# Performance work log

Measured on AMD Instinct MI355X. Metric: run time of the kernel, lower is better.

Reference implementation:

```python
import jax, jax.numpy as jnp
import numpy as np

N_DEV, N_TASK, E = 50000, 100000, 1000000
F_DEV, F_TASK = 64, 64
HID, H, OUT = 16, 4, 32
L1 = HID * H  # 64


def gat_conv(x_src, x_dst, src, dst, W_src, W_dst, a_src, a_dst, b, heads, ch, n_dst):
    """PyG-style bipartite GATConv (concat=True, negative_slope=0.2, no self loops)."""
    hs = (x_src @ W_src).reshape(-1, heads, ch)          # [Ns,H,C]
    hd = (x_dst @ W_dst).reshape(-1, heads, ch)          # [Nd,H,C]
    al_s = jnp.sum(hs * a_src, axis=-1)                  # [Ns,H]
    al_d = jnp.sum(hd * a_dst, axis=-1)                  # [Nd,H]
    e = jax.nn.leaky_relu(al_s[src] + al_d[dst], 0.2)    # [E,H]
    m = jax.ops.segment_max(e, dst, num_segments=n_dst)  # [Nd,H]
    ex = jnp.exp(e - m[dst])
    den = jax.ops.segment_sum(ex, dst, num_segments=n_dst)
    attn = ex / (den[dst] + 1e-16)                       # [E,H]
    msg = attn[:, :, None] * hs[src]                     # [E,H,C]
    out = jax.ops.segment_sum(msg, dst, num_segments=n_dst)
    return out.reshape(n_dst, heads * ch) + b


def setup_inputs() -> dict:
    key = jax.random.key(0)
    ks = jax.random.split(key, 32)
    rn = lambda k, s: jax.random.normal(k, s, jnp.float32) * 0.1
    inp = {
        "x_dev": jax.random.normal(ks[0], (N_DEV, F_DEV), jnp.float32),
        "x_task": jax.random.normal(ks[1], (N_TASK, F_TASK), jnp.float32),
        "writes_src": jax.random.randint(ks[2], (E,), 0, N_DEV, jnp.int32),
        "writes_dst": jax.random.randint(ks[3], (E,), 0, N_TASK, jnp.int32),
        "wb_src": jax.random.randint(ks[4], (E,), 0, N_TASK, jnp.int32),
        "wb_dst": jax.random.randint(ks[5], (E,), 0, N_DEV, jnp.int32),
        # layer1: dev->task (src=dev, dst=task), H=4, C=16
        "W1a_src": rn(ks[6], (F_DEV, L1)), "W1a_dst": rn(ks[7], (F_TASK, L1)),
        "a1a_src": rn(ks[8], (H, HID)), "a1a_dst": rn(ks[9], (H, HID)),
        "b1a": jnp.zeros((L1,), jnp.float32),
        # layer1: task->dev
        "W1b_src": rn(ks[10], (F_TASK, L1)), "W1b_dst": rn(ks[11], (F_DEV, L1)),
        "a1b_src": rn(ks[12], (H, HID)), "a1b_dst": rn(ks[13], (H, HID)),
        "b1b": jnp.zeros((L1,), jnp.float32),
        # layer2: dev->task, heads=1, C=32
        "W2a_src": rn(ks[14], (L1, OUT)), "W2a_dst": rn(ks[15], (L1, OUT)),
        "a2a_src": rn(ks[16], (1, OUT)), "a2a_dst": rn(ks[17], (1, OUT)),
        "b2a": jnp.zeros((OUT,), jnp.float32),
        # layer2: task->dev
        "W2b_src": rn(ks[18], (L1, OUT)), "W2b_dst": rn(ks[19], (L1, OUT)),
        "a2b_src": rn(ks[20], (1, OUT)), "a2b_dst": rn(ks[21], (1, OUT)),
        "b2b": jnp.zeros((OUT,), jnp.float32),
    }
    return inp


def reference(x_dev, x_task, writes_src, writes_dst, wb_src, wb_dst,
              W1a_src, W1a_dst, a1a_src, a1a_dst, b1a,
              W1b_src, W1b_dst, a1b_src, a1b_dst, b1b,
              W2a_src, W2a_dst, a2a_src, a2a_dst, b2a,
              W2b_src, W2b_dst, a2b_src, a2b_dst, b2b):
    x_task_1 = jax.nn.relu(gat_conv(x_dev, x_task, writes_src, writes_dst,
                                    W1a_src, W1a_dst, a1a_src, a1a_dst, b1a, H, HID, N_TASK))
    x_dev_1 = jax.nn.relu(gat_conv(x_task, x_dev, wb_src, wb_dst,
                                   W1b_src, W1b_dst, a1b_src, a1b_dst, b1b, H, HID, N_DEV))
    x_task_2 = jax.nn.relu(gat_conv(x_dev_1, x_task_1, writes_src, writes_dst,
                                    W2a_src, W2a_dst, a2a_src, a2a_dst, b2a, 1, OUT, N_TASK))
    x_dev_2 = jax.nn.relu(gat_conv(x_task_1, x_dev_1, wb_src, wb_dst,
                                   W2b_src, W2b_dst, a2b_src, a2b_dst, b2b, 1, OUT, N_DEV))
    return (x_dev_2, x_task_2)
```

## Files before the change

kernel.cpp:

```cpp
#include <hip/hip_runtime.h>
#include <math.h>

#define NDEV 50000
#define NTASK 100000
#define NE 1000000
#define NBK 98
#define SH_T 10
#define SH_D 9
#define NBLK_AB 512
#define CHUNK ((NE + NBLK_AB - 1) / NBLK_AB)

typedef unsigned int uint;

__device__ inline uint bf16rn(float f) {
    uint x = __float_as_uint(f);
    return (x + 0x7fffu + ((x >> 16) & 1u)) >> 16;
}
__device__ inline uint bf16pair(float a, float b) {
    return bf16rn(a) | (bf16rn(b) << 16);
}
__device__ inline float blo(uint p) { return __uint_as_float(p << 16); }
__device__ inline float bhi(uint p) { return __uint_as_float(p & 0xffff0000u); }

__global__ void prep_weights(
    const float* __restrict__ W1a_src, const float* __restrict__ a1a_src,
    const float* __restrict__ W1a_dst, const float* __restrict__ a1a_dst,
    const float* __restrict__ W1b_src, const float* __restrict__ a1b_src,
    const float* __restrict__ W1b_dst, const float* __restrict__ a1b_dst,
    const float* __restrict__ W2a_src, const float* __restrict__ a2a_src,
    const float* __restrict__ W2a_dst, const float* __restrict__ a2a_dst,
    const float* __restrict__ W2b_src, const float* __restrict__ a2b_src,
    const float* __restrict__ W2b_dst, const float* __restrict__ a2b_dst,
    float* __restrict__ Whd1_0, float* __restrict__ Whd1_1,
    float* __restrict__ Wht1_0, float* __restrict__ Wht1_1,
    float* __restrict__ Whd2_0, float* __restrict__ Whd2_1,
    float* __restrict__ Wht2_0, float* __restrict__ Wht2_1)
{
    int f = threadIdx.x;
    if (f >= 64) return;
    for (int c = 0; c < 32; ++c) Whd1_0[f*36 + c] = W1a_src[f*64 + c];
    for (int h = 0; h < 4; ++h) {
        float s = 0.f;
        for (int c = 0; c < 16; ++c) s += W1a_src[f*64 + h*16 + c] * a1a_src[h*16 + c];
        Whd1_0[f*36 + 32 + h] = s;
    }
    for (int c = 0; c < 32; ++c) Whd1_1[f*36 + c] = W1a_src[f*64 + 32 + c];
    for (int h = 0; h < 4; ++h) {
        float s = 0.f;
        for (int c = 0; c < 16; ++c) s += W1b_dst[f*64 + h*16 + c] * a1b_dst[h*16 + c];
        Whd1_1[f*36 + 32 + h] = s;
    }
    for (int c = 0; c < 32; ++c) Wht1_0[f*36 + c] = W1b_src[f*64 + c];
    for (int h = 0; h < 4; ++h) {
        float s = 0.f;
        for (int c = 0; c < 16; ++c) s += W1b_src[f*64 + h*16 + c] * a1b_src[h*16 + c];
        Wht1_0[f*36 + 32 + h] = s;
    }
    for (int c = 0; c < 32; ++c) Wht1_1[f*36 + c] = W1b_src[f*64 + 32 + c];
    for (int h = 0; h < 4; ++h) {
        float s = 0.f;
        for (int c = 0; c < 16; ++c) s += W1a_dst[f*64 + h*16 + c] * a1a_dst[h*16 + c];
        Wht1_1[f*36 + 32 + h] = s;
    }
    for (int c = 0; c < 16; ++c) Whd2_0[f*20 + c] = W2a_src[f*32 + c];
    { float s = 0.f; for (int c = 0; c < 32; ++c) s += W2a_src[f*32+c]*a2a_src[c]; Whd2_0[f*20+16] = s; }
    Whd2_0[f*20+17] = 0.f; Whd2_0[f*20+18] = 0.f; Whd2_0[f*20+19] = 0.f;
    for (int c = 0; c < 16; ++c) Whd2_1[f*20 + c] = W2a_src[f*32 + 16 + c];
    { float s = 0.f; for (int c = 0; c < 32; ++c) s += W2b_dst[f*32+c]*a2b_dst[c]; Whd2_1[f*20+16] = s; }
    Whd2_1[f*20+17] = 0.f; Whd2_1[f*20+18] = 0.f; Whd2_1[f*20+19] = 0.f;
    for (int c = 0; c < 16; ++c) Wht2_0[f*20 + c] = W2b_src[f*32 + c];
    { float s = 0.f; for (int c = 0; c < 32; ++c) s += W2b_src[f*32+c]*a2b_src[c]; Wht2_0[f*20+16] = s; }
    Wht2_0[f*20+17] = 0.f; Wht2_0[f*20+18] = 0.f; Wht2_0[f*20+19] = 0.f;
    for (int c = 0; c < 16; ++c) Wht2_1[f*20 + c] = W2b_src[f*32 + 16 + c];
    { float s = 0.f; for (int c = 0; c < 32; ++c) s += W2a_dst[f*32+c]*a2a_dst[c]; Wht2_1[f*20+16] = s; }
    Wht2_1[f*20+17] = 0.f; Wht2_1[f*20+18] = 0.f; Wht2_1[f*20+19] = 0.f;
}

template<int COP, int CHS, int NA, int AST, int HSTR>
__device__ __forceinline__ void gemm_half_block(
    const float* __restrict__ X, int N, const float* __restrict__ Wc,
    uint* __restrict__ hs, float* __restrict__ aout,
    int n0, int hsoff, float* w)
{
    for (int i = threadIdx.x; i < 64 * COP; i += 256) w[i] = Wc[i];
    __syncthreads();
    int n = n0 + threadIdx.x;
    if (n >= N) return;

    const float4* X4 = reinterpret_cast<const float4*>(X + (size_t)n * 64);
    float4 acc[CHS/4];
    #pragma unroll
    for (int j = 0; j < CHS/4; ++j) acc[j] = make_float4(0.f, 0.f, 0.f, 0.f);
    float aacc[NA];
    #pragma unroll
    for (int j = 0; j < NA; ++j) aacc[j] = 0.f;

    for (int k16 = 0; k16 < 4; ++k16) {
        float4 xv4[4];
        #pragma unroll
        for (int q = 0; q < 4; ++q) xv4[q] = X4[k16*4 + q];
        float xs[16];
        #pragma unroll
        for (int q = 0; q < 4; ++q) {
            xs[4*q+0] = xv4[q].x; xs[4*q+1] = xv4[q].y;
            xs[4*q+2] = xv4[q].z; xs[4*q+3] = xv4[q].w;
        }
        #pragma unroll
        for (int kk = 0; kk < 16; ++kk) {
            int k = k16*16 + kk;
            float xv = xs[kk];
            const float* wr = &w[k * COP];
            #pragma unroll
            for (int j = 0; j < CHS/4; ++j) {
                float4 wv = *reinterpret_cast<const float4*>(wr + 4*j);
                acc[j].x += xv * wv.x; acc[j].y += xv * wv.y;
                acc[j].z += xv * wv.z; acc[j].w += xv * wv.w;
            }
            #pragma unroll
            for (int j = 0; j < NA; ++j) aacc[j] += xv * wr[CHS + j];
        }
    }
    uint pk[CHS/2];
    #pragma unroll
    for (int j = 0; j < CHS/4; ++j) {
        pk[2*j]   = bf16pair(acc[j].x, acc[j].y);
        pk[2*j+1] = bf16pair(acc[j].z, acc[j].w);
    }
    uint4* hrow = reinterpret_cast<uint4*>(hs + (size_t)n * HSTR + hsoff);
    #pragma unroll
    for (int j = 0; j < CHS/8; ++j)
        hrow[j] = make_uint4(pk[4*j], pk[4*j+1], pk[4*j+2], pk[4*j+3]);
    #pragma unroll
    for (int j = 0; j < NA; ++j) aout[(size_t)n*AST + j] = aacc[j];
}

template<int COP, int CHS, int NA, int AST, int HSTR>
__device__ __forceinline__ void gemm_half_block_b16(
    const uint* __restrict__ X, int N, const float* __restrict__ Wc,
    uint* __restrict__ hs, float* __restrict__ aout,
    int n0, int hsoff, float* w)
{
    for (int i = threadIdx.x; i < 64 * COP; i += 256) w[i] = Wc[i];
    __syncthreads();
    int n = n0 + threadIdx.x;
    if (n >= N) return;

    const uint4* X4 = reinterpret_cast<const uint4*>(X + (size_t)n * 32);
    float4 acc[CHS/4];
    #pragma unroll
    for (int j = 0; j < CHS/4; ++j) acc[j] = make_float4(0.f, 0.f, 0.f, 0.f);
    float aacc[NA];
    #pragma unroll
    for (int j = 0; j < NA; ++j) aacc[j] = 0.f;

    for (int k16 = 0; k16 < 4; ++k16) {
        uint4 u0 = X4[2*k16], u1 = X4[2*k16 + 1];
        float xs[16];
        xs[0] = blo(u0.x); xs[1] = bhi(u0.x); xs[2] = blo(u0.y); xs[3] = bhi(u0.y);
        xs[4] = blo(u0.z); xs[5] = bhi(u0.z); xs[6] = blo(u0.w); xs[7] = bhi(u0.w);
        xs[8] = blo(u1.x); xs[9] = bhi(u1.x); xs[10] = blo(u1.y); xs[11] = bhi(u1.y);
        xs[12] = blo(u1.z); xs[13] = bhi(u1.z); xs[14] = blo(u1.w); xs[15] = bhi(u1.w);
        #pragma unroll
        for (int kk = 0; kk < 16; ++kk) {
            int k = k16*16 + kk;
            float xv = xs[kk];
            const float* wr = &w[k * COP];
            #pragma unroll
            for (int j = 0; j < CHS/4; ++j) {
                float4 wv = *reinterpret_cast<const float4*>(wr + 4*j);
                acc[j].x += xv * wv.x; acc[j].y += xv * wv.y;
                acc[j].z += xv * wv.z; acc[j].w += xv * wv.w;
            }
            #pragma unroll
            for (int j = 0; j < NA; ++j) aacc[j] += xv * wr[CHS + j];
        }
    }
    uint pk[CHS/2];
    #pragma unroll
    for (int j = 0; j < CHS/4; ++j) {
        pk[2*j]   = bf16pair(acc[j].x, acc[j].y);
        pk[2*j+1] = bf16pair(acc[j].z, acc[j].w);
    }
    uint4* hrow = reinterpret_cast<uint4*>(hs + (size_t)n * HSTR + hsoff);
    #pragma unroll
    for (int j = 0; j < CHS/8; ++j)
        hrow[j] = make_uint4(pk[4*j], pk[4*j+1], pk[4*j+2], pk[4*j+3]);
    #pragma unroll
    for (int j = 0; j < NA; ++j) aout[(size_t)n*AST + j] = aacc[j];
}

template<int COP, int CHS, int NA, int AST, int HSTR>
__global__ __launch_bounds__(256, 4) void gemm_quad(
    const float* __restrict__ XA, int NrA,
    const float* __restrict__ WcA0, const float* __restrict__ WcA1,
    uint* __restrict__ hsA, float* __restrict__ alsA, float* __restrict__ aldA,
    const float* __restrict__ XB, int NrB,
    const float* __restrict__ WcB0, const float* __restrict__ WcB1,
    uint* __restrict__ hsB, float* __restrict__ alsB, float* __restrict__ aldB)
{
    __shared__ __align__(16) float w[64 * COP];
    int nbA = (NrA + 255) / 256;
    int nbB = (NrB + 255) / 256;
    int nbHalf = nbA + nbB;
    int b = (int)blockIdx.x;
    int half = b >= nbHalf ? 1 : 0;
    if (half) b -= nbHalf;
    int isB = b >= nbA ? 1 : 0;
    if (isB) b -= nbA;
    const float* X = isB ? XB : XA;
    int N = isB ? NrB : NrA;
    const float* Wc = isB ? (half ? WcB1 : WcB0) : (half ? WcA1 : WcA0);
    uint* hs = isB ? hsB : hsA;
    float* aout = isB ? (half ? aldB : alsB) : (half ? aldA : alsA);
    gemm_half_block<COP, CHS, NA, AST, HSTR>(X, N, Wc, hs, aout, b * 256, half * (CHS/2), w);
}

template<int COP, int CHS, int NA, int AST, int HSTR>
__global__ __launch_bounds__(256, 4) void gemm_quad_b16(
    const uint* __restrict__ XA, int NrA,
    const float* __restrict__ WcA0, const float* __restrict__ WcA1,
    uint* __restrict__ hsA, float* __restrict__ alsA, float* __restrict__ aldA,
    const uint* __restrict__ XB, int NrB,
    const float* __restrict__ WcB0, const float* __restrict__ WcB1,
    uint* __restrict__ hsB, float* __restrict__ alsB, float* __restrict__ aldB)
{
    __shared__ __align__(16) float w[64 * COP];
    int nbA = (NrA + 255) / 256;
    int nbB = (NrB + 255) / 256;
    int nbHalf = nbA + nbB;
    int b = (int)blockIdx.x;
    int half = b >= nbHalf ? 1 : 0;
    if (half) b -= nbHalf;
    int isB = b >= nbA ? 1 : 0;
    if (isB) b -= nbA;
    const uint* X = isB ? XB : XA;
    int N = isB ? NrB : NrA;
    const float* Wc = isB ? (half ? WcB1 : WcB0) : (half ? WcA1 : WcA0);
    uint* hs = isB ? hsB : hsA;
    float* aout = isB ? (half ? aldB : alsB) : (half ? aldA : alsA);
    gemm_half_block_b16<COP, CHS, NA, AST, HSTR>(X, N, Wc, hs, aout, b * 256, half * (CHS/2), w);
}

__global__ __launch_bounds__(256) void bucketA(
    const int* __restrict__ wdst, const int* __restrict__ bdst,
    int* __restrict__ bh_t, int* __restrict__ bh_d)
{
    __shared__ int lh[128];
    int dir = (int)blockIdx.x >= NBLK_AB;
    int blk = (int)blockIdx.x - (dir ? NBLK_AB : 0);
    const int* dst = dir ? bdst : wdst;
    int sh = dir ? SH_D : SH_T;
    int* bh = dir ? bh_d : bh_t;
    for (int i = threadIdx.x; i < 128; i += 256) lh[i] = 0;
    __syncthreads();
    int e0 = blk * CHUNK, e1 = min(NE, e0 + CHUNK);
    for (int i = e0 + threadIdx.x; i < e1; i += 256)
        atomicAdd(&lh[dst[i] >> sh], 1);
    __syncthreads();
    if (threadIdx.x < NBK) bh[threadIdx.x * NBLK_AB + blk] = lh[threadIdx.x];
}

__global__ __launch_bounds__(256) void scanB1(
    int* __restrict__ bh_t, int* __restrict__ bh_d, int* __restrict__ rowtot)
{
    __shared__ int sm[256];
    int b = blockIdx.x;
    int dir = b >= NBK;
    int row = dir ? b - NBK : b;
    int* bh = dir ? bh_d : bh_t;
    int t = threadIdx.x;
    int base = row * NBLK_AB;
    int v0 = bh[base + 2*t], v1 = bh[base + 2*t + 1];
    int s = v0 + v1;
    sm[t] = s; __syncthreads();
    int x = s;
    for (int off = 1; off < 256; off <<= 1) {
        int y = (t >= off) ? sm[t - off] : 0;
        __syncthreads();
        x += y; sm[t] = x;
        __syncthreads();
    }
    int run = x - s;
    bh[base + 2*t] = run;
    bh[base + 2*t + 1] = run + v0;
    if (t == 255) rowtot[b] = x;
}

__global__ void scanB2(const int* __restrict__ rowtot,
                       int* __restrict__ coarse_t, int* __restrict__ coarse_d,
                       int* __restrict__ offs_task, int* __restrict__ offs_dev)
{
    __shared__ int sm[256];
    int t = threadIdx.x;
    int v = (t < NBK) ? rowtot[t] : 0;
    sm[t] = v; __syncthreads();
    int x = v;
    for (int off = 1; off < 256; off <<= 1) {
        int y = (t >= off) ? sm[t - off] : 0;
        __syncthreads();
        x += y; sm[t] = x;
        __syncthreads();
    }
    if (t < NBK) coarse_t[t] = x - v;
    __syncthreads();
    int v2 = (t < NBK) ? rowtot[NBK + t] : 0;
    sm[t] = v2; __syncthreads();
    int x2 = v2;
    for (int off = 1; off < 256; off <<= 1) {
        int y = (t >= off) ? sm[t - off] : 0;
        __syncthreads();
        x2 += y; sm[t] = x2;
        __syncthreads();
    }
    if (t < NBK) coarse_d[t] = x2 - v2;
    if (t == 0) {
        coarse_t[NBK] = NE; coarse_d[NBK] = NE;
        offs_task[NTASK] = NE; offs_dev[NDEV] = NE;
    }
}

__global__ __launch_bounds__(256) void bucketB(
    const int* __restrict__ wsrc, const int* __restrict__ wdst,
    const int* __restrict__ bsrc, const int* __restrict__ bdst,
    const int* __restrict__ bh_t, const int* __restrict__ bh_d,
    const int* __restrict__ coarse_t, const int* __restrict__ coarse_d,
    uint* __restrict__ pairs_w, uint* __restrict__ pairs_b)
{
    __shared__ int cur[128];
    int dir = (int)blockIdx.x >= NBLK_AB;
    int blk = (int)blockIdx.x - (dir ? NBLK_AB : 0);
    const int* src = dir ? bsrc : wsrc;
    const int* dst = dir ? bdst : wdst;
    int sh = dir ? SH_D : SH_T;
    uint msk = (1u << sh) - 1u;
    const int* bh = dir ? bh_d : bh_t;
    const int* coarse = dir ? coarse_d : coarse_t;
    uint* pairs = dir ? pairs_b : pairs_w;
    if (threadIdx.x < NBK)
        cur[threadIdx.x] = bh[threadIdx.x * NBLK_AB + blk] + coarse[threadIdx.x];
    __syncthreads();
    int e0 = blk * CHUNK, e1 = min(NE, e0 + CHUNK);
    for (int i = e0 + threadIdx.x; i < e1; i += 256) {
        int d = dst[i];
        int pos = atomicAdd(&cur[d >> sh], 1);
        pairs[pos] = (uint)src[i] | (((uint)d & msk) << 20);
    }
}

__global__ __launch_bounds__(256) void bucketC(
    const uint* __restrict__ pairs_w, const int* __restrict__ coarse_t,
    int* __restrict__ offs_task, int* __restrict__ s_w,
    const uint* __restrict__ pairs_b, const int* __restrict__ coarse_d,
    int* __restrict__ offs_dev, int* __restrict__ s_b)
{
    __shared__ int loff[1024];
    __shared__ int sm[256];
    int dir = (int)blockIdx.x >= NBK;
    int bkt = (int)blockIdx.x - (dir ? NBK : 0);
    const uint* pairs = dir ? pairs_b : pairs_w;
    const int* coarse = dir ? coarse_d : coarse_t;
    int* offs = dir ? offs_dev : offs_task;
    int* sarr = dir ? s_b : s_w;
    int sh = dir ? SH_D : SH_T;
    int rng = 1 << sh;
    int d0 = bkt << sh;
    int N = dir ? NDEV : NTASK;
    int dcnt = min(rng, N - d0);
    int e0 = coarse[bkt], e1 = coarse[bkt + 1];
    int t = threadIdx.x;
    for (int i = t; i < rng; i += 256) loff[i] = 0;
    __syncthreads();
    for (int i = e0 + t; i < e1; i += 256)
        atomicAdd(&loff[pairs[i] >> 20], 1);
    __syncthreads();
    int per = rng >> 8;
    int v[4]; int s = 0;
    for (int k = 0; k < per; ++k) { v[k] = loff[t * per + k]; s += v[k]; }
    sm[t] = s;
    __syncthreads();
    int x = s;
    for (int off = 1; off < 256; off <<= 1) {
        int y = (t >= off) ? sm[t - off] : 0;
        __syncthreads();
        x += y; sm[t] = x;
        __syncthreads();
    }
    int run = e0 + x - s;
    for (int k = 0; k < per; ++k) {
        int dl = t * per + k;
        loff[dl] = run;
        if (dl < dcnt) offs[d0 + dl] = run;
        run += v[k];
    }
    __syncthreads();
    for (int i = e0 + t; i < e1; i += 256) {
        uint u = pairs[i];
        int pos = atomicAdd(&loff[u >> 20], 1);
        sarr[pos] = (int)(u & 0xFFFFFu);
    }
}

__global__ __launch_bounds__(256) void gat_agg_l1(
    const int* __restrict__ offs_t, const int* __restrict__ srcs_t,
    const float* __restrict__ als_d_, const float* __restrict__ ald_t,
    const uint* __restrict__ hs_d_, const float* __restrict__ bias_a, uint* __restrict__ out_t,
    const int* __restrict__ offs_d, const int* __restrict__ srcs_d,
    const float* __restrict__ als_t, const float* __restrict__ ald_d,
    const uint* __restrict__ hs_t, const float* __restrict__ bias_b, uint* __restrict__ out_d)
{
    const int nbT = (NTASK + 3) / 4;
    int wave = threadIdx.x >> 6, lane = threadIdx.x & 63;
    const int* offs; const int* srcs; const float* als; const float* ald;
    const uint* hs; const float* bias; uint* out; int Nd, d;
    if ((int)blockIdx.x < nbT) {
        offs = offs_t; srcs = srcs_t; als = als_d_; ald = ald_t; hs = hs_d_;
        bias = bias_a; out = out_t; Nd = NTASK; d = blockIdx.x * 4 + wave;
    } else {
        offs = offs_d; srcs = srcs_d; als = als_t; ald = ald_d; hs = hs_t;
        bias = bias_b; out = out_d; Nd = NDEV; d = ((int)blockIdx.x - nbT) * 4 + wave;
    }
    if (d >= Nd) return;
    int sub = lane >> 3;
    int cl  = lane & 7;
    int h   = cl >> 1;
    float aldv = ald[d * 4 + h];
    int beg = __builtin_amdgcn_readfirstlane(offs[d]);
    int end = __builtin_amdgcn_readfirstlane(offs[d + 1]);
    float denA = 0.f, a0A = 0.f, a1A = 0.f, a2A = 0.f, a3A = 0.f,
          a4A = 0.f, a5A = 0.f, a6A = 0.f, a7A = 0.f;
    float denB = 0.f, a0B = 0.f, a1B = 0.f, a2B = 0.f, a3B = 0.f,
          a4B = 0.f, a5B = 0.f, a6B = 0.f, a7B = 0.f;
    int iA = beg + sub, iB = beg + sub + 8;
    int sA = srcs[iA < end ? iA : beg];
    int sB = srcs[iB < end ? iB : beg];
    for (; iA < end; ) {
        int iA2 = iA + 16, iB2 = iB + 16;
        int sA2 = srcs[iA2 < end ? iA2 : beg];
        int sB2 = srcs[iB2 < end ? iB2 : beg];
        bool vB = iB < end;
        float eA = als[sA * 4 + h] + aldv; eA = fmaxf(eA, 0.2f * eA);
        float eB = als[sB * 4 + h] + aldv; eB = fmaxf(eB, 0.2f * eB);
        float wA = __expf(eA);
        float wB = vB ? __expf(eB) : 0.f;
        uint4 pA = *reinterpret_cast<const uint4*>(hs + sA * 32 + 4 * cl);
        uint4 pB = *reinterpret_cast<const uint4*>(hs + sB * 32 + 4 * cl);
        denA += wA;
        a0A += wA * blo(pA.x); a1A += wA * bhi(pA.x);
        a2A += wA * blo(pA.y); a3A += wA * bhi(pA.y);
        a4A += wA * blo(pA.z); a5A += wA * bhi(pA.z);
        a6A += wA * blo(pA.w); a7A += wA * bhi(pA.w);
        denB += wB;
        a0B += wB * blo(pB.x); a1B += wB * bhi(pB.x);
        a2B += wB * blo(pB.y); a3B += wB * bhi(pB.y);
        a4B += wB * blo(pB.z); a5B += wB * bhi(pB.z);
        a6B += wB * blo(pB.w); a7B += wB * bhi(pB.w);
        iA = iA2; iB = iB2; sA = sA2; sB = sB2;
    }
    float den = denA + denB;
    float a0 = a0A + a0B, a1 = a1A + a1B, a2 = a2A + a2B, a3 = a3A + a3B;
    float a4 = a4A + a4B, a5 = a5A + a5B, a6 = a6A + a6B, a7 = a7A + a7B;
    den += __shfl_xor(den, 8, 64); den += __shfl_xor(den, 16, 64); den += __shfl_xor(den, 32, 64);
    a0 += __shfl_xor(a0, 8, 64); a0 += __shfl_xor(a0, 16, 64); a0 += __shfl_xor(a0, 32, 64);
    a1 += __shfl_xor(a1, 8, 64); a1 += __shfl_xor(a1, 16, 64); a1 += __shfl_xor(a1, 32, 64);
    a2 += __shfl_xor(a2, 8, 64); a2 += __shfl_xor(a2, 16, 64); a2 += __shfl_xor(a2, 32, 64);
    a3 += __shfl_xor(a3, 8, 64); a3 += __shfl_xor(a3, 16, 64); a3 += __shfl_xor(a3, 32, 64);
    a4 += __shfl_xor(a4, 8, 64); a4 += __shfl_xor(a4, 16, 64); a4 += __shfl_xor(a4, 32, 64);
    a5 += __shfl_xor(a5, 8, 64); a5 += __shfl_xor(a5, 16, 64); a5 += __shfl_xor(a5, 32, 64);
    a6 += __shfl_xor(a6, 8, 64); a6 += __shfl_xor(a6, 16, 64); a6 += __shfl_xor(a6, 32, 64);
    a7 += __shfl_xor(a7, 8, 64); a7 += __shfl_xor(a7, 16, 64); a7 += __shfl_xor(a7, 32, 64);
    if (lane < 8) {
        float inv = 1.f / (den + 1e-16f);
        float o0 = fmaxf(a0 * inv + bias[8*cl + 0], 0.f);
        float o1 = fmaxf(a1 * inv + bias[8*cl + 1], 0.f);
        float o2 = fmaxf(a2 * inv + bias[8*cl + 2], 0.f);
        float o3 = fmaxf(a3 * inv + bias[8*cl + 3], 0.f);
        float o4 = fmaxf(a4 * inv + bias[8*cl + 4], 0.f);
        float o5 = fmaxf(a5 * inv + bias[8*cl + 5], 0.f);
        float o6 = fmaxf(a6 * inv + bias[8*cl + 6], 0.f);
        float o7 = fmaxf(a7 * inv + bias[8*cl + 7], 0.f);
        uint4 pk;
        pk.x = bf16pair(o0, o1);
        pk.y = bf16pair(o2, o3);
        pk.z = bf16pair(o4, o5);
        pk.w = bf16pair(o6, o7);
        *reinterpret_cast<uint4*>(&out[(size_t)d * 32 + 4*cl]) = pk;
    }
}

__global__ __launch_bounds__(256) void gat_agg_l2(
    const int* __restrict__ offs_t, const int* __restrict__ srcs_t,
    const float* __restrict__ als_d_, const float* __restrict__ ald_t,
    const uint* __restrict__ hs_d_, const float* __restrict__ bias_a, float* __restrict__ out_t,
    const int* __restrict__ offs_d, const int* __restrict__ srcs_d,
    const float* __restrict__ als_t, const float* __restrict__ ald_d,
    const uint* __restrict__ hs_t, const float* __restrict__ bias_b, float* __restrict__ out_d)
{
    const int nbT = (NTASK + 3) / 4;
    int wave = threadIdx.x >> 6, lane = threadIdx.x & 63;
    const int* offs; const int* srcs; const float* als; const float* ald;
    const uint* hs; const float* bias; float* out; int Nd, d;
    if ((int)blockIdx.x < nbT) {
        offs = offs_t; srcs = srcs_t; als = als_d_; ald = ald_t; hs = hs_d_;
        bias = bias_a; out = out_t; Nd = NTASK; d = blockIdx.x * 4 + wave;
    } else {
        offs = offs_d; srcs = srcs_d; als = als_t; ald = ald_d; hs = hs_t;
        bias = bias_b; out = out_d; Nd = NDEV; d = ((int)blockIdx.x - nbT) * 4 + wave;
    }
    if (d >= Nd) return;
    int sub = lane >> 3;
    int cl  = lane & 7;
    float aldv = ald[d];
    int beg = __builtin_amdgcn_readfirstlane(offs[d]);
    int end = __builtin_amdgcn_readfirstlane(offs[d + 1]);
    float denA = 0.f, a0A = 0.f, a1A = 0.f, a2A = 0.f, a3A = 0.f;
    float denB = 0.f, a0B = 0.f, a1B = 0.f, a2B = 0.f, a3B = 0.f;
    float denC = 0.f, a0C = 0.f, a1C = 0.f, a2C = 0.f, a3C = 0.f;
    float denD = 0.f, a0D = 0.f, a1D = 0.f, a2D = 0.f, a3D = 0.f;
    for (int i0 = beg + sub; i0 < end; i0 += 32) {
        int iB = i0 + 8, iC = i0 + 16, iD = i0 + 24;
        bool vB = iB < end, vC = iC < end, vD = iD < end;
        int sA = srcs[i0];
        int sB = srcs[vB ? iB : beg];
        int sC = srcs[vC ? iC : beg];
        int sD = srcs[vD ? iD : beg];
        float eA = als[sA] + aldv; eA = fmaxf(eA, 0.2f * eA);
        float eB = als[sB] + aldv; eB = fmaxf(eB, 0.2f * eB);
        float eC = als[sC] + aldv; eC = fmaxf(eC, 0.2f * eC);
        float eD = als[sD] + aldv; eD = fmaxf(eD, 0.2f * eD);
        float wA = __expf(eA);
        float wB = vB ? __expf(eB) : 0.f;
        float wC = vC ? __expf(eC) : 0.f;
        float wD = vD ? __expf(eD) : 0.f;
        uint2 pA = *reinterpret_cast<const uint2*>(hs + sA * 16 + 2 * cl);
        uint2 pB = *reinterpret_cast<const uint2*>(hs + sB * 16 + 2 * cl);
        uint2 pC = *reinterpret_cast<const uint2*>(hs + sC * 16 + 2 * cl);
        uint2 pD = *reinterpret_cast<const uint2*>(hs + sD * 16 + 2 * cl);
        denA += wA;
        a0A += wA * blo(pA.x); a1A += wA * bhi(pA.x);
        a2A += wA * blo(pA.y); a3A += wA * bhi(pA.y);
        denB += wB;
        a0B += wB * blo(pB.x); a1B += wB * bhi(pB.x);
        a2B += wB * blo(pB.y); a3B += wB * bhi(pB.y);
        denC += wC;
        a0C += wC * blo(pC.x); a1C += wC * bhi(pC.x);
        a2C += wC * blo(pC.y); a3C += wC * bhi(pC.y);
        denD += wD;
        a0D += wD * blo(pD.x); a1D += wD * bhi(pD.x);
        a2D += wD * blo(pD.y); a3D += wD * bhi(pD.y);
    }
    float den = (denA + denB) + (denC + denD);
    float a0 = (a0A + a0B) + (a0C + a0D);
    float a1 = (a1A + a1B) + (a1C + a1D);
    float a2 = (a2A + a2B) + (a2C + a2D);
    float a3 = (a3A + a3B) + (a3C + a3D);
    den += __shfl_xor(den, 8, 64); den += __shfl_xor(den, 16, 64); den += __shfl_xor(den, 32, 64);
    a0  += __shfl_xor(a0, 8, 64);  a0  += __shfl_xor(a0, 16, 64);  a0  += __shfl_xor(a0, 32, 64);
    a1  += __shfl_xor(a1, 8, 64);  a1  += __shfl_xor(a1, 16, 64);  a1  += __shfl_xor(a1, 32, 64);
    a2  += __shfl_xor(a2, 8, 64);  a2  += __shfl_xor(a2, 16, 64);  a2  += __shfl_xor(a2, 32, 64);
    a3  += __shfl_xor(a3, 8, 64);  a3  += __shfl_xor(a3, 16, 64);  a3  += __shfl_xor(a3, 32, 64);
    if (lane < 8) {
        float inv = 1.f / (den + 1e-16f);
        float4 o;
        o.x = fmaxf(a0 * inv + bias[4*cl + 0], 0.f);
        o.y = fmaxf(a1 * inv + bias[4*cl + 1], 0.f);
        o.z = fmaxf(a2 * inv + bias[4*cl + 2], 0.f);
        o.w = fmaxf(a3 * inv + bias[4*cl + 3], 0.f);
        *reinterpret_cast<float4*>(&out[(size_t)d * 32 + 4*cl]) = o;
    }
}

extern "C" void kernel_launch(void* const* d_in, const int* in_sizes, int n_in,
                              void* d_out, int out_size, void* d_ws, size_t ws_size,
                              hipStream_t stream)
{
    const float* x_dev   = (const float*)d_in[0];
    const float* x_task  = (const float*)d_in[1];
    const int* writes_src = (const int*)d_in[2];
    const int* writes_dst = (const int*)d_in[3];
    const int* wb_src     = (const int*)d_in[4];
    const int* wb_dst     = (const int*)d_in[5];
    const float* W1a_src = (const float*)d_in[6],  *W1a_dst = (const float*)d_in[7];
    const float* a1a_src = (const float*)d_in[8],  *a1a_dst = (const float*)d_in[9];
    const float* b1a     = (const float*)d_in[10];
    const float* W1b_src = (const float*)d_in[11], *W1b_dst = (const float*)d_in[12];
    const float* a1b_src = (const float*)d_in[13], *a1b_dst = (const float*)d_in[14];
    const float* b1b     = (const float*)d_in[15];
    const float* W2a_src = (const float*)d_in[16], *W2a_dst = (const float*)d_in[17];
    const float* a2a_src = (const float*)d_in[18], *a2a_dst = (const float*)d_in[19];
    const float* b2a     = (const float*)d_in[20];
    const float* W2b_src = (const float*)d_in[21], *W2b_dst = (const float*)d_in[22];
    const float* a2b_src = (const float*)d_in[23], *a2b_dst = (const float*)d_in[24];
    const float* b2b     = (const float*)d_in[25];

    float* out_dev2  = (float*)d_out;
    float* out_task2 = (float*)d_out + (size_t)NDEV * 32;

    char* ws = (char*)d_ws;
    size_t off = 0;
    auto take = [&](size_t bytes) -> void* {
        off = (off + 255) & ~(size_t)255;
        void* p = ws + off; off += bytes; return p;
    };
    int* s_w       = (int*)take((size_t)NE * 4);
    int* s_b       = (int*)take((size_t)NE * 4);
    int* offs_task = (int*)take((size_t)(NTASK + 1) * 4);
    int* offs_dev  = (int*)take((size_t)(NDEV + 1) * 4);
    int* bh_t      = (int*)take((size_t)NBK * NBLK_AB * 4);
    int* bh_d      = (int*)take((size_t)NBK * NBLK_AB * 4);
    int* coarse_t  = (int*)take((size_t)(NBK + 1) * 4);
    int* coarse_d  = (int*)take((size_t)(NBK + 1) * 4);
    int* rowtot    = (int*)take(256 * 4);
    float* Whd1_0  = (float*)take(64 * 36 * 4);
    float* Whd1_1  = (float*)take(64 * 36 * 4);
    float* Wht1_0  = (float*)take(64 * 36 * 4);
    float* Wht1_1  = (float*)take(64 * 36 * 4);
    float* Whd2_0  = (float*)take(64 * 20 * 4);
    float* Whd2_1  = (float*)take(64 * 20 * 4);
    float* Wht2_0  = (float*)take(64 * 20 * 4);
    float* Wht2_1  = (float*)take(64 * 20 * 4);
    uint* hs_dev    = (uint*)take((size_t)NDEV * 32 * 4);
    float* als_dev  = (float*)take((size_t)NDEV * 4 * 4);
    float* aldx_dev = (float*)take((size_t)NDEV * 4 * 4);
    uint* hs_task   = (uint*)take((size_t)NTASK * 32 * 4);
    float* als_task = (float*)take((size_t)NTASK * 4 * 4);
    float* aldx_task= (float*)take((size_t)NTASK * 4 * 4);
    uint* x_task1   = (uint*)take((size_t)NTASK * 32 * 4);
    uint* x_dev1    = (uint*)take((size_t)NDEV * 32 * 4);
    uint* pairs_w = (uint*)x_task1;
    uint* pairs_b = pairs_w + NE;
    (void)ws_size; (void)n_in; (void)in_sizes; (void)out_size;

    prep_weights<<<1, 64, 0, stream>>>(
        W1a_src, a1a_src, W1a_dst, a1a_dst, W1b_src, a1b_src, W1b_dst, a1b_dst,
        W2a_src, a2a_src, W2a_dst, a2a_dst, W2b_src, a2b_src, W2b_dst, a2b_dst,
        Whd1_0, Whd1_1, Wht1_0, Wht1_1, Whd2_0, Whd2_1, Wht2_0, Wht2_1);

    bucketA<<<2 * NBLK_AB, 256, 0, stream>>>(writes_dst, wb_dst, bh_t, bh_d);
    scanB1<<<2 * NBK, 256, 0, stream>>>(bh_t, bh_d, rowtot);
    scanB2<<<1, 256, 0, stream>>>(rowtot, coarse_t, coarse_d, offs_task, offs_dev);
    bucketB<<<2 * NBLK_AB, 256, 0, stream>>>(writes_src, writes_dst, wb_src, wb_dst,
                                             bh_t, bh_d, coarse_t, coarse_d, pairs_w, pairs_b);
    bucketC<<<2 * NBK, 256, 0, stream>>>(pairs_w, coarse_t, offs_task, s_w,
                                         pairs_b, coarse_d, offs_dev, s_b);

    int nbHalf = (NDEV + 255) / 256 + (NTASK + 255) / 256;
    gemm_quad<36, 32, 4, 4, 32><<<2 * nbHalf, 256, 0, stream>>>(
        x_dev, NDEV, Whd1_0, Whd1_1, hs_dev, als_dev, aldx_dev,
        x_task, NTASK, Wht1_0, Wht1_1, hs_task, als_task, aldx_task);

    int nbagg = (NTASK + 3) / 4 + (NDEV + 3) / 4;
    gat_agg_l1<<<nbagg, 256, 0, stream>>>(
        offs_task, s_w, als_dev, aldx_task, hs_dev, b1a, x_task1,
        offs_dev, s_b, als_task, aldx_dev, hs_task, b1b, x_dev1);

    gemm_quad_b16<20, 16, 1, 1, 16><<<2 * nbHalf, 256, 0, stream>>>(
        x_dev1, NDEV, Whd2_0, Whd2_1, hs_dev, als_dev, aldx_dev,
        x_task1, NTASK, Wht2_0, Wht2_1, hs_task, als_task, aldx_task);

    gat_agg_l2<<<nbagg, 256, 0, stream>>>(
        offs_task, s_w, als_dev, aldx_task, hs_dev, b2a, out_task2,
        offs_dev, s_b, als_task, aldx_dev, hs_task, b2b, out_dev2);
}
```

Measured before the change: 240.1 us.

## Replace multi-pass counting sort with fixed-capacity bucket scatter using global atomics

Replaces the five-kernel CSR build (histogram, two scans, scatter, per-bucket sort) with two kernels. Each block stages its edge chunk in shared memory, reserves space in fixed-capacity global buckets through one atomic per bucket, and scatters into them. The second kernel then sorts each bucket locally and emits per-node offsets plus degree arrays, which the aggregation kernels now use instead of offs[d+1]. This removes three launches and a global prefix scan. The cost is that it assumes no bucket receives more than CAP edges, which holds for near-uniform destinations but would silently overflow on skewed graphs, and it adds a memset and extra workspace.

```diff
diff --git a/kernel.cpp b/kernel.cpp
--- a/kernel.cpp
+++ b/kernel.cpp
@@ -4,9 +4,10 @@
 #define NDEV 50000
 #define NTASK 100000
 #define NE 1000000
-#define NBK 98
-#define SH_T 10
-#define SH_D 9
+#define NBK2 196
+#define SH_T2 9
+#define SH_D2 8
+#define CAP 6144
 #define NBLK_AB 512
 #define CHUNK ((NE + NBLK_AB - 1) / NBLK_AB)
 
@@ -241,38 +242,81 @@
     gemm_half_block_b16<COP, CHS, NA, AST, HSTR>(X, N, Wc, hs, aout, b * 256, half * (CHS/2), w);
 }
 
-__global__ __launch_bounds__(256) void bucketA(
-    const int* __restrict__ wdst, const int* __restrict__ bdst,
-    int* __restrict__ bh_t, int* __restrict__ bh_d)
-{
-    __shared__ int lh[128];
+__global__ __launch_bounds__(256) void bucketB2(
+    const int* __restrict__ wsrc, const int* __restrict__ wdst,
+    const int* __restrict__ bsrc, const int* __restrict__ bdst,
+    int* __restrict__ cntb_t, int* __restrict__ cntb_d,
+    uint* __restrict__ pairs_w, uint* __restrict__ pairs_b)
+{
+    __shared__ uint lpair[CHUNK];
+    __shared__ unsigned short lbkt[CHUNK];
+    __shared__ int lcnt[NBK2], lbase[NBK2];
     int dir = (int)blockIdx.x >= NBLK_AB;
     int blk = (int)blockIdx.x - (dir ? NBLK_AB : 0);
+    const int* src = dir ? bsrc : wsrc;
     const int* dst = dir ? bdst : wdst;
-    int sh = dir ? SH_D : SH_T;
-    int* bh = dir ? bh_d : bh_t;
-    for (int i = threadIdx.x; i < 128; i += 256) lh[i] = 0;
-    __syncthreads();
-    int e0 = blk * CHUNK, e1 = min(NE, e0 + CHUNK);
-    for (int i = e0 + threadIdx.x; i < e1; i += 256)
-        atomicAdd(&lh[dst[i] >> sh], 1);
-    __syncthreads();
-    if (threadIdx.x < NBK) bh[threadIdx.x * NBLK_AB + blk] = lh[threadIdx.x];
-}
-
-__global__ __launch_bounds__(256) void scanB1(
-    int* __restrict__ bh_t, int* __restrict__ bh_d, int* __restrict__ rowtot)
-{
+    int sh = dir ? SH_D2 : SH_T2;
+    uint msk = (1u << sh) - 1u;
+    int* cntb = dir ? cntb_d : cntb_t;
+    uint* pairs = dir ? pairs_b : pairs_w;
+    int t = threadIdx.x;
+    for (int i = t; i < NBK2; i += 256) lcnt[i] = 0;
+    __syncthreads();
+    int e0 = blk * CHUNK, e1 = min(NE, e0 + CHUNK), n = e1 - e0;
+    for (int i = t; i < n; i += 256) {
+        int d = dst[e0 + i];
+        int b = d >> sh;
+        lpair[i] = (uint)src[e0 + i] | (((uint)d & msk) << 20);
+        lbkt[i] = (unsigned short)b;
+        atomicAdd(&lcnt[b], 1);
+    }
+    __syncthreads();
+    for (int i = t; i < NBK2; i += 256) {
+        int c = lcnt[i];
+        lbase[i] = c ? atomicAdd(&cntb[i], c) : 0;
+        lcnt[i] = 0;
+    }
+    __syncthreads();
+    for (int i = t; i < n; i += 256) {
+        int b = lbkt[i];
+        int r = atomicAdd(&lcnt[b], 1);
+        pairs[(size_t)b * CAP + lbase[b] + r] = lpair[i];
+    }
+}
+
+__global__ __launch_bounds__(256) void bucketC2(
+    const uint* __restrict__ pairs_w, const int* __restrict__ cntb_t,
+    int* __restrict__ offs_t, int* __restrict__ deg_t, int* __restrict__ s_w,
+    const uint* __restrict__ pairs_b, const int* __restrict__ cntb_d,
+    int* __restrict__ offs_d, int* __restrict__ deg_d, int* __restrict__ s_b)
+{
+    __shared__ int loff[512];
     __shared__ int sm[256];
-    int b = blockIdx.x;
-    int dir = b >= NBK;
-    int row = dir ? b - NBK : b;
-    int* bh = dir ? bh_d : bh_t;
+    int dir = (int)blockIdx.x >= NBK2;
+    int bkt = (int)blockIdx.x - (dir ? NBK2 : 0);
+    const uint* pairs = dir ? pairs_b : pairs_w;
+    const int* cntb = dir ? cntb_d : cntb_t;
+    int* offs = dir ? offs_d : offs_t;
+    int* deg  = dir ? deg_d  : deg_t;
+    int* sarr = dir ? s_b : s_w;
+    int sh = dir ? SH_D2 : SH_T2;
+    int rng = 1 << sh;
+    int d0 = bkt << sh;
+    int N = dir ? NDEV : NTASK;
+    int dcnt = min(rng, N - d0);
+    int e0 = bkt * CAP;
+    int cnt = cntb[bkt];
     int t = threadIdx.x;
-    int base = row * NBLK_AB;
-    int v0 = bh[base + 2*t], v1 = bh[base + 2*t + 1];
-    int s = v0 + v1;
-    sm[t] = s; __syncthreads();
+    for (int i = t; i < rng; i += 256) loff[i] = 0;
+    __syncthreads();
+    for (int i = t; i < cnt; i += 256)
+        atomicAdd(&loff[pairs[e0 + i] >> 20], 1);
+    __syncthreads();
+    int per = rng >> 8;
+    int v[2]; int s = 0;
+    for (int k = 0; k < per; ++k) { v[k] = loff[t * per + k]; s += v[k]; }
+    sm[t] = s;
+    __syncthreads();
     int x = s;
     for (int off = 1; off < 256; off <<= 1) {
         int y = (t >= off) ? sm[t - off] : 0;
@@ -280,143 +324,38 @@
         x += y; sm[t] = x;
         __syncthreads();
     }
-    int run = x - s;
-    bh[base + 2*t] = run;
-    bh[base + 2*t + 1] = run + v0;
-    if (t == 255) rowtot[b] = x;
-}
-
-__global__ void scanB2(const int* __restrict__ rowtot,
-                       int* __restrict__ coarse_t, int* __restrict__ coarse_d,
-                       int* __restrict__ offs_task, int* __restrict__ offs_dev)
-{
-    __shared__ int sm[256];
-    int t = threadIdx.x;
-    int v = (t < NBK) ? rowtot[t] : 0;
-    sm[t] = v; __syncthreads();
-    int x = v;
-    for (int off = 1; off < 256; off <<= 1) {
-        int y = (t >= off) ? sm[t - off] : 0;
-        __syncthreads();
-        x += y; sm[t] = x;
-        __syncthreads();
-    }
-    if (t < NBK) coarse_t[t] = x - v;
-    __syncthreads();
-    int v2 = (t < NBK) ? rowtot[NBK + t] : 0;
-    sm[t] = v2; __syncthreads();
-    int x2 = v2;
-    for (int off = 1; off < 256; off <<= 1) {
-        int y = (t >= off) ? sm[t - off] : 0;
-        __syncthreads();
-        x2 += y; sm[t] = x2;
-        __syncthreads();
-    }
-    if (t < NBK) coarse_d[t] = x2 - v2;
-    if (t == 0) {
-        coarse_t[NBK] = NE; coarse_d[NBK] = NE;
-        offs_task[NTASK] = NE; offs_dev[NDEV] = NE;
-    }
-}
-
-__global__ __launch_bounds__(256) void bucketB(
-    const int* __restrict__ wsrc, const int* __restrict__ wdst,
-    const int* __restrict__ bsrc, const int* __restrict__ bdst,
-    const int* __restrict__ bh_t, const int* __restrict__ bh_d,
-    const int* __restrict__ coarse_t, const int* __restrict__ coarse_d,
-    uint* __restrict__ pairs_w, uint* __restrict__ pairs_b)
-{
-    __shared__ int cur[128];
-    int dir = (int)blockIdx.x >= NBLK_AB;
-    int blk = (int)blockIdx.x - (dir ? NBLK_AB : 0);
-    const int* src = dir ? bsrc : wsrc;
-    const int* dst = dir ? bdst : wdst;
-    int sh = dir ? SH_D : SH_T;
-    uint msk = (1u << sh) - 1u;
-    const int* bh = dir ? bh_d : bh_t;
-    const int* coarse = dir ? coarse_d : coarse_t;
-    uint* pairs = dir ? pairs_b : pairs_w;
-    if (threadIdx.x < NBK)
-        cur[threadIdx.x] = bh[threadIdx.x * NBLK_AB + blk] + coarse[threadIdx.x];
-    __syncthreads();
-    int e0 = blk * CHUNK, e1 = min(NE, e0 + CHUNK);
-    for (int i = e0 + threadIdx.x; i < e1; i += 256) {
-        int d = dst[i];
-        int pos = atomicAdd(&cur[d >> sh], 1);
-        pairs[pos] = (uint)src[i] | (((uint)d & msk) << 20);
-    }
-}
-
-__global__ __launch_bounds__(256) void bucketC(
-    const uint* __restrict__ pairs_w, const int* __restrict__ coarse_t,
-    int* __restrict__ offs_task, int* __restrict__ s_w,
-    const uint* __restrict__ pairs_b, const int* __restrict__ coarse_d,
-    int* __restrict__ offs_dev, int* __restrict__ s_b)
-{
-    __shared__ int loff[1024];
-    __shared__ int sm[256];
-    int dir = (int)blockIdx.x >= NBK;
-    int bkt = (int)blockIdx.x - (dir ? NBK : 0);
-    const uint* pairs = dir ? pairs_b : pairs_w;
-    const int* coarse = dir ? coarse_d : coarse_t;
-    int* offs = dir ? offs_dev : offs_task;
-    int* sarr = dir ? s_b : s_w;
-    int sh = dir ? SH_D : SH_T;
-    int rng = 1 << sh;
-    int d0 = bkt << sh;
-    int N = dir ? NDEV : NTASK;
-    int dcnt = min(rng, N - d0);
-    int e0 = coarse[bkt], e1 = coarse[bkt + 1];
-    int t = threadIdx.x;
-    for (int i = t; i < rng; i += 256) loff[i] = 0;
-    __syncthreads();
-    for (int i = e0 + t; i < e1; i += 256)
-        atomicAdd(&loff[pairs[i] >> 20], 1);
-    __syncthreads();
-    int per = rng >> 8;
-    int v[4]; int s = 0;
-    for (int k = 0; k < per; ++k) { v[k] = loff[t * per + k]; s += v[k]; }
-    sm[t] = s;
-    __syncthreads();
-    int x = s;
-    for (int off = 1; off < 256; off <<= 1) {
-        int y = (t >= off) ? sm[t - off] : 0;
-        __syncthreads();
-        x += y; sm[t] = x;
-        __syncthreads();
-    }
     int run = e0 + x - s;
     for (int k = 0; k < per; ++k) {
         int dl = t * per + k;
         loff[dl] = run;
-        if (dl < dcnt) offs[d0 + dl] = run;
+        if (dl < dcnt) { offs[d0 + dl] = run; deg[d0 + dl] = v[k]; }
         run += v[k];
     }
     __syncthreads();
-    for (int i = e0 + t; i < e1; i += 256) {
-        uint u = pairs[i];
+    for (int i = t; i < cnt; i += 256) {
+        uint u = pairs[e0 + i];
         int pos = atomicAdd(&loff[u >> 20], 1);
         sarr[pos] = (int)(u & 0xFFFFFu);
     }
 }
 
 __global__ __launch_bounds__(256) void gat_agg_l1(
-    const int* __restrict__ offs_t, const int* __restrict__ srcs_t,
+    const int* __restrict__ offs_t, const int* __restrict__ deg_t, const int* __restrict__ srcs_t,
     const float* __restrict__ als_d_, const float* __restrict__ ald_t,
     const uint* __restrict__ hs_d_, const float* __restrict__ bias_a, uint* __restrict__ out_t,
-    const int* __restrict__ offs_d, const int* __restrict__ srcs_d,
+    const int* __restrict__ offs_d, const int* __restrict__ deg_d, const int* __restrict__ srcs_d,
     const float* __restrict__ als_t, const float* __restrict__ ald_d,
     const uint* __restrict__ hs_t, const float* __restrict__ bias_b, uint* __restrict__ out_d)
 {
     const int nbT = (NTASK + 3) / 4;
     int wave = threadIdx.x >> 6, lane = threadIdx.x & 63;
-    const int* offs; const int* srcs; const float* als; const float* ald;
+    const int* offs; const int* degp; const int* srcs; const float* als; const float* ald;
     const uint* hs; const float* bias; uint* out; int Nd, d;
     if ((int)blockIdx.x < nbT) {
-        offs = offs_t; srcs = srcs_t; als = als_d_; ald = ald_t; hs = hs_d_;
+        offs = offs_t; degp = deg_t; srcs = srcs_t; als = als_d_; ald = ald_t; hs = hs_d_;
         bias = bias_a; out = out_t; Nd = NTASK; d = blockIdx.x * 4 + wave;
     } else {
-        offs = offs_d; srcs = srcs_d; als = als_t; ald = ald_d; hs = hs_t;
+        offs = offs_d; degp = deg_d; srcs = srcs_d; als = als_t; ald = ald_d; hs = hs_t;
         bias = bias_b; out = out_d; Nd = NDEV; d = ((int)blockIdx.x - nbT) * 4 + wave;
     }
     if (d >= Nd) return;
@@ -425,7 +364,7 @@
     int h   = cl >> 1;
     float aldv = ald[d * 4 + h];
     int beg = __builtin_amdgcn_readfirstlane(offs[d]);
-    int end = __builtin_amdgcn_readfirstlane(offs[d + 1]);
+    int end = beg + __builtin_amdgcn_readfirstlane(degp[d]);
     float denA = 0.f, a0A = 0.f, a1A = 0.f, a2A = 0.f, a3A = 0.f,
           a4A = 0.f, a5A = 0.f, a6A = 0.f, a7A = 0.f;
     float denB = 0.f, a0B = 0.f, a1B = 0.f, a2B = 0.f, a3B = 0.f,
@@ -488,22 +427,22 @@
 }
 
 __global__ __launch_bounds__(256) void gat_agg_l2(
-    const int* __restrict__ offs_t, const int* __restrict__ srcs_t,
+    const int* __restrict__ offs_t, const int* __restrict__ deg_t, const int* __restrict__ srcs_t,
     const float* __restrict__ als_d_, const float* __restrict__ ald_t,
     const uint* __restrict__ hs_d_, const float* __restrict__ bias_a, float* __restrict__ out_t,
-    const int* __restrict__ offs_d, const int* __restrict__ srcs_d,
+    const int* __restrict__ offs_d, const int* __restrict__ deg_d, const int* __restrict__ srcs_d,
     const float* __restrict__ als_t, const float* __restrict__ ald_d,
     const uint* __restrict__ hs_t, const float* __restrict__ bias_b, float* __restrict__ out_d)
 {
     const int nbT = (NTASK + 3) / 4;
     int wave = threadIdx.x >> 6, lane = threadIdx.x & 63;
-    const int* offs; const int* srcs; const float* als; const float* ald;
+    const int* offs; const int* degp; const int* srcs; const float* als; const float* ald;
     const uint* hs; const float* bias; float* out; int Nd, d;
     if ((int)blockIdx.x < nbT) {
-        offs = offs_t; srcs = srcs_t; als = als_d_; ald = ald_t; hs = hs_d_;
+        offs = offs_t; degp = deg_t; srcs = srcs_t; als = als_d_; ald = ald_t; hs = hs_d_;
         bias = bias_a; out = out_t; Nd = NTASK; d = blockIdx.x * 4 + wave;
     } else {
-        offs = offs_d; srcs = srcs_d; als = als_t; ald = ald_d; hs = hs_t;
+        offs = offs_d; degp = deg_d; srcs = srcs_d; als = als_t; ald = ald_d; hs = hs_t;
         bias = bias_b; out = out_d; Nd = NDEV; d = ((int)blockIdx.x - nbT) * 4 + wave;
     }
     if (d >= Nd) return;
@@ -511,7 +450,7 @@
     int cl  = lane & 7;
     float aldv = ald[d];
     int beg = __builtin_amdgcn_readfirstlane(offs[d]);
-    int end = __builtin_amdgcn_readfirstlane(offs[d + 1]);
+    int end = beg + __builtin_amdgcn_readfirstlane(degp[d]);
     float denA = 0.f, a0A = 0.f, a1A = 0.f, a2A = 0.f, a3A = 0.f;
     float denB = 0.f, a0B = 0.f, a1B = 0.f, a2B = 0.f, a3B = 0.f;
     float denC = 0.f, a0C = 0.f, a1C = 0.f, a2C = 0.f, a3C = 0.f;
@@ -601,15 +540,16 @@
         off = (off + 255) & ~(size_t)255;
         void* p = ws + off; off += bytes; return p;
     };
-    int* s_w       = (int*)take((size_t)NE * 4);
-    int* s_b       = (int*)take((size_t)NE * 4);
-    int* offs_task = (int*)take((size_t)(NTASK + 1) * 4);
-    int* offs_dev  = (int*)take((size_t)(NDEV + 1) * 4);
-    int* bh_t      = (int*)take((size_t)NBK * NBLK_AB * 4);
-    int* bh_d      = (int*)take((size_t)NBK * NBLK_AB * 4);
-    int* coarse_t  = (int*)take((size_t)(NBK + 1) * 4);
-    int* coarse_d  = (int*)take((size_t)(NBK + 1) * 4);
-    int* rowtot    = (int*)take(256 * 4);
+    const size_t SREG = (size_t)NBK2 * CAP;
+    int* s_w       = (int*)take(SREG * 4);
+    int* s_b       = (int*)take(SREG * 4);
+    int* offs_task = (int*)take((size_t)NTASK * 4);
+    int* offs_dev  = (int*)take((size_t)NDEV * 4);
+    int* deg_task  = (int*)take((size_t)NTASK * 4);
+    int* deg_dev   = (int*)take((size_t)NDEV * 4);
+    int* cntb      = (int*)take((size_t)2 * NBK2 * 4);
+    int* cntb_t    = cntb;
+    int* cntb_d    = cntb + NBK2;
     float* Whd1_0  = (float*)take(64 * 36 * 4);
     float* Whd1_1  = (float*)take(64 * 36 * 4);
     float* Wht1_0  = (float*)take(64 * 36 * 4);
@@ -627,21 +567,20 @@
     uint* x_task1   = (uint*)take((size_t)NTASK * 32 * 4);
     uint* x_dev1    = (uint*)take((size_t)NDEV * 32 * 4);
     uint* pairs_w = (uint*)x_task1;
-    uint* pairs_b = pairs_w + NE;
+    uint* pairs_b = pairs_w + SREG;
     (void)ws_size; (void)n_in; (void)in_sizes; (void)out_size;
+
+    hipMemsetAsync(cntb, 0, (size_t)2 * NBK2 * 4, stream);
 
     prep_weights<<<1, 64, 0, stream>>>(
         W1a_src, a1a_src, W1a_dst, a1a_dst, W1b_src, a1b_src, W1b_dst, a1b_dst,
         W2a_src, a2a_src, W2a_dst, a2a_dst, W2b_src, a2b_src, W2b_dst, a2b_dst,
         Whd1_0, Whd1_1, Wht1_0, Wht1_1, Whd2_0, Whd2_1, Wht2_0, Wht2_1);
 
-    bucketA<<<2 * NBLK_AB, 256, 0, stream>>>(writes_dst, wb_dst, bh_t, bh_d);
-    scanB1<<<2 * NBK, 256, 0, stream>>>(bh_t, bh_d, rowtot);
-    scanB2<<<1, 256, 0, stream>>>(rowtot, coarse_t, coarse_d, offs_task, offs_dev);
-    bucketB<<<2 * NBLK_AB, 256, 0, stream>>>(writes_src, writes_dst, wb_src, wb_dst,
-                                             bh_t, bh_d, coarse_t, coarse_d, pairs_w, pairs_b);
-    bucketC<<<2 * NBK, 256, 0, stream>>>(pairs_w, coarse_t, offs_task, s_w,
-                                         pairs_b, coarse_d, offs_dev, s_b);
+    bucketB2<<<2 * NBLK_AB, 256, 0, stream>>>(writes_src, writes_dst, wb_src, wb_dst,
+                                              cntb_t, cntb_d, pairs_w, pairs_b);
+    bucketC2<<<2 * NBK2, 256, 0, stream>>>(pairs_w, cntb_t, offs_task, deg_task, s_w,
+                                           pairs_b, cntb_d, offs_dev, deg_dev, s_b);
 
     int nbHalf = (NDEV + 255) / 256 + (NTASK + 255) / 256;
     gemm_quad<36, 32, 4, 4, 32><<<2 * nbHalf, 256, 0, stream>>>(
@@ -650,14 +589,14 @@
 
     int nbagg = (NTASK + 3) / 4 + (NDEV + 3) / 4;
     gat_agg_l1<<<nbagg, 256, 0, stream>>>(
-        offs_task, s_w, als_dev, aldx_task, hs_dev, b1a, x_task1,
-        offs_dev, s_b, als_task, aldx_dev, hs_task, b1b, x_dev1);
+        offs_task, deg_task, s_w, als_dev, aldx_task, hs_dev, b1a, x_task1,
+        offs_dev, deg_dev, s_b, als_task, aldx_dev, hs_task, b1b, x_dev1);
 
     gemm_quad_b16<20, 16, 1, 1, 16><<<2 * nbHalf, 256, 0, stream>>>(
         x_dev1, NDEV, Whd2_0, Whd2_1, hs_dev, als_dev, aldx_dev,
         x_task1, NTASK, Wht2_0, Wht2_1, hs_task, als_task, aldx_task);
 
     gat_agg_l2<<<nbagg, 256, 0, stream>>>(
-        offs_task, s_w, als_dev, aldx_task, hs_dev, b2a, out_task2,
-        offs_dev, s_b, als_task, aldx_dev, hs_task, b2b, out_dev2);
-}
+        offs_task, deg_task, s_w, als_dev, aldx_task, hs_dev, b2a, out_task2,
+        offs_dev, deg_dev, s_b, als_task, aldx_dev, hs_task, b2b, out_dev2);
+}
```

Result: no change. 240.6 us (+0.2%).
